# Kernel optimization log

Measured on AMD Instinct MI355X. Metric: run time of the kernel, lower is better.

The kernel has to match this reference:

```python
import jax, jax.numpy as jnp
import numpy as np

B, D, H, DH, NQ, NK = 64, 768, 8, 128, 256, 256


def _ln(x, g, b, eps=1e-5):
    m = x.mean(-1, keepdims=True)
    v = ((x - m) ** 2).mean(-1, keepdims=True)
    return (x - m) / jnp.sqrt(v + eps) * g + b


def setup_inputs() -> dict:
    key = jax.random.key(0)
    ks = jax.random.split(key, 16)
    w = lambda k, s: jax.random.normal(k, s, jnp.float32) * 0.02
    return {
        'emb_cause': jax.random.normal(ks[0], (B, D), jnp.float32),
        'emb_action': jax.random.normal(ks[1], (B, D), jnp.float32),
        'tok_cause': jax.random.normal(ks[2], (B, NK, D), jnp.float32),
        'tok_effect': jax.random.normal(ks[3], (B, NQ, D), jnp.float32),
        'fuse_ln_g': jnp.ones(2 * D), 'fuse_ln_b': jnp.zeros(2 * D),
        'fuse_w1': w(ks[4], (2 * D, D)), 'fuse_b1': jnp.zeros(D),
        'fuse_w2': w(ks[5], (D, D)), 'fuse_b2': jnp.zeros(D),
        'delta_ln_g': jnp.ones(D), 'delta_ln_b': jnp.zeros(D),
        'delta_w': w(ks[6], (D, D)), 'delta_b': jnp.zeros(D),
        'qg_w': w(ks[7], (D, H * DH)), 'qg_b': jnp.zeros(H * DH),
        'kg_w': w(ks[8], (D, H * DH)), 'kg_b': jnp.zeros(H * DH),
        'eff_ln_g': jnp.ones(D), 'eff_ln_b': jnp.zeros(D),
        'eff_w1': w(ks[9], (D, D)), 'eff_b1': jnp.zeros(D),
        'eff_w2': w(ks[10], (D, D)), 'eff_b2': jnp.zeros(D),
        'u_w': w(ks[11], (D, H * DH)),
        'v_w': w(ks[12], (D, H * DH)),
        'logit_scale': jnp.zeros(()),
    }


def reference(emb_cause, emb_action, tok_cause, tok_effect,
              fuse_ln_g, fuse_ln_b, fuse_w1, fuse_b1, fuse_w2, fuse_b2,
              delta_ln_g, delta_ln_b, delta_w, delta_b,
              qg_w, qg_b, kg_w, kg_b,
              eff_ln_g, eff_ln_b, eff_w1, eff_b1, eff_w2, eff_b2,
              u_w, v_w, logit_scale):
    # fuse: LN -> Linear -> GELU(exact) -> Linear (dropout = identity, eval)
    ctx_in = jnp.concatenate([emb_cause, emb_action], axis=-1)  # (B, 2D)
    h = jax.nn.gelu(_ln(ctx_in, fuse_ln_g, fuse_ln_b) @ fuse_w1 + fuse_b1, approximate=False)
    ctx = h @ fuse_w2 + fuse_b2  # (B, D)

    delta_e = _ln(ctx, delta_ln_g, delta_ln_b) @ delta_w + delta_b  # (B, D)
    pooled_effect = tok_effect.mean(axis=1)  # (B, D)
    e_shifted = pooled_effect + delta_e

    eh = jax.nn.gelu(_ln(ctx, eff_ln_g, eff_ln_b) @ eff_w1 + eff_b1, approximate=False)
    effect_pred = eh @ eff_w2 + eff_b2  # (B, D)

    q_gate = 1.0 + jnp.tanh(jax.nn.silu(ctx @ qg_w + qg_b)).reshape(B, H, DH)
    k_gate = 1.0 + jnp.tanh(jax.nn.silu(ctx @ kg_w + kg_b)).reshape(B, H, DH)

    # logit bias: torch code materializes (B,H,Nq,Nk,Dh); equivalent math is a
    # per-head inner product u.v (independent of q) broadcast over Nq.
    u = (e_shifted @ u_w).reshape(B, H, DH)            # (B, H, Dh)
    v = (tok_cause @ v_w).reshape(B, NK, H, DH)        # (B, Nk, H, Dh)
    bias = jnp.einsum('bhd,bkhd->bhk', u, v) / np.float32(np.sqrt(DH))
    logit_bias = jnp.exp(logit_scale) * jnp.broadcast_to(bias[:, :, None, :], (B, H, NQ, NK))

    return (q_gate, k_gate, e_shifted, delta_e, logit_bias, effect_pred)
```

## Files before the change

kernel.cpp:

```cpp
#include <hip/hip_runtime.h>
#include <math.h>

#define TPB 256

typedef float vf4 __attribute__((ext_vector_type(4)));

__device__ __forceinline__ float gelu_f(float x) {
    return 0.5f * x * (1.0f + erff(x * 0.70710678118654752f));
}
__device__ __forceinline__ float gate_f(float x) {
    float si = x / (1.0f + expf(-x));
    return 1.0f + tanhf(si);
}

template <class XL>
__device__ __forceinline__ void gemm_tile(XL xload, const float* __restrict__ W, int Wld, int cb,
                                          int k0, int kslice, float* part, int totN, int gcol, int s,
                                          float* __restrict__ xs, float* __restrict__ wt)
{
    const int t = threadIdx.x;
    const int tr4 = (t >> 4) << 2;
    const int tc4 = (t & 15) << 2;
    const int a  = t >> 5, kk = t & 31;
    const int wk = t >> 6, wc = t & 63;
    float xv[8], wv[8];
#pragma unroll
    for (int j = 0; j < 8; ++j) {
        xv[j] = xload(a + 8 * j, k0 + kk);
        wv[j] = W[(size_t)(k0 + wk + 4 * j) * Wld + cb + wc];
    }
    float acc[4][4] = {{0.f,0.f,0.f,0.f},{0.f,0.f,0.f,0.f},{0.f,0.f,0.f,0.f},{0.f,0.f,0.f,0.f}};
    for (int kc = 0; kc < kslice; kc += 32) {
#pragma unroll
        for (int j = 0; j < 8; ++j) {
            xs[kk * 68 + a + 8 * j] = xv[j];
            wt[(wk + 4 * j) * 68 + wc] = wv[j];
        }
        __syncthreads();
        int kn = kc + 32;
        if (kn < kslice) {
#pragma unroll
            for (int j = 0; j < 8; ++j) {
                xv[j] = xload(a + 8 * j, k0 + kn + kk);
                wv[j] = W[(size_t)(k0 + kn + wk + 4 * j) * Wld + cb + wc];
            }
        }
#pragma unroll
        for (int k = 0; k < 32; ++k) {
            float4 xq = *(const float4*)&xs[k * 68 + tr4];
            float4 wq = *(const float4*)&wt[k * 68 + tc4];
            acc[0][0] += xq.x * wq.x; acc[0][1] += xq.x * wq.y; acc[0][2] += xq.x * wq.z; acc[0][3] += xq.x * wq.w;
            acc[1][0] += xq.y * wq.x; acc[1][1] += xq.y * wq.y; acc[1][2] += xq.y * wq.z; acc[1][3] += xq.y * wq.w;
            acc[2][0] += xq.z * wq.x; acc[2][1] += xq.z * wq.y; acc[2][2] += xq.z * wq.z; acc[2][3] += xq.z * wq.w;
            acc[3][0] += xq.w * wq.x; acc[3][1] += xq.w * wq.y; acc[3][2] += xq.w * wq.z; acc[3][3] += xq.w * wq.w;
        }
        __syncthreads();
    }
    float* pp = part + (size_t)(s * 64 + tr4) * totN + gcol + tc4;
#pragma unroll
    for (int i = 0; i < 4; ++i)
#pragma unroll
        for (int j = 0; j < 4; ++j)
            pp[i * totN + j] = acc[i][j];
}

#define GEMM_LDS __shared__ float xs[32 * 68]; __shared__ float wt[32 * 68];

__device__ __forceinline__ void pool_task(const float* __restrict__ tok_effect,
                                          float* __restrict__ pp, int m, int t)
{
    int cch = m % 3, b = (m / 3) % 64, qz = m / 192;
    int c = cch * TPB + t;
    const float* base = tok_effect + (size_t)(b * 256 + qz * 64) * 768 + c;
    float s = 0.f;
#pragma unroll 16
    for (int q = 0; q < 64; ++q) s += __builtin_nontemporal_load(base + (size_t)q * 768);
    pp[(qz * 64 + b) * 768 + c] = s;
}

struct G1Args {
    const float *ec, *ea, *flg, *flb, *w1;
    const float *tok_effect;
    float *part1, *pp;
};
__global__ __launch_bounds__(256) void k_g1(G1Args A)
{
    GEMM_LDS;
    __shared__ float sred[8][64];
    __shared__ float sst[128];
    const int t = threadIdx.x;
    if (blockIdx.x >= 144) {
        pool_task(A.tok_effect, A.pp, blockIdx.x - 144, t);
        return;
    }
    {
        int row = t & 63, part = t >> 6;
        const float* src = (part < 2) ? (A.ec + row * 768 + part * 384)
                                      : (A.ea + row * 768 + (part - 2) * 384);
        const vf4* s4 = (const vf4*)src;
        float sum = 0.f, sq = 0.f;
#pragma unroll 8
        for (int j = 0; j < 96; ++j) {
            vf4 v = s4[j];
            sum += v.x + v.y + v.z + v.w;
            sq  += v.x * v.x + v.y * v.y + v.z * v.z + v.w * v.w;
        }
        sred[part][row] = sum;
        sred[4 + part][row] = sq;
        __syncthreads();
        if (t < 64) {
            float s = sred[0][t] + sred[1][t] + sred[2][t] + sred[3][t];
            float q = sred[4][t] + sred[5][t] + sred[6][t] + sred[7][t];
            float mean = s * (1.f / 1536.f);
            float var = q * (1.f / 1536.f) - mean * mean;
            sst[2 * t]     = mean;
            sst[2 * t + 1] = rsqrtf(var + 1e-5f);
        }
        __syncthreads();
    }
    int ct = blockIdx.x % 12, s = blockIdx.x / 12;
    auto xl = [&](int r, int k) {
        float raw = (k < 768) ? A.ec[r * 768 + k] : A.ea[r * 768 + (k - 768)];
        return (raw - sst[2 * r]) * sst[2 * r + 1] * A.flg[k] + A.flb[k];
    };
    gemm_tile(xl, A.w1, 768, ct * 64, s * 128, 128, A.part1, 768, ct * 64, s, xs, wt);
}

struct G2Args {
    const float *part1, *b1, *w2;
    const float *tok_effect;
    float *part2, *pp;
};
__global__ __launch_bounds__(256) void k_g2(G2Args A)
{
    GEMM_LDS;
    if (blockIdx.x >= 144) {
        pool_task(A.tok_effect, A.pp, blockIdx.x - 144 + 384, threadIdx.x);
        return;
    }
    int ct = blockIdx.x % 12, s = blockIdx.x / 12;
    auto xl = [&](int r, int k) {
        float v = A.b1[k];
#pragma unroll
        for (int q = 0; q < 12; ++q) v += A.part1[(size_t)(q * 64 + r) * 768 + k];
        return gelu_f(v);
    };
    gemm_tile(xl, A.w2, 768, ct * 64, s * 64, 64, A.part2, 768, ct * 64, s, xs, wt);
}

__global__ __launch_bounds__(256) void k_ln(const float* __restrict__ part2, const float* __restrict__ b2,
                                            float* __restrict__ ctx, float* __restrict__ stats2)
{
    int r = blockIdx.x, t = threadIdx.x;
    __shared__ float red[4];
    float v[3]; float sum = 0.f;
#pragma unroll
    for (int j = 0; j < 3; ++j) {
        int c = t + j * TPB;
        float x = b2[c];
#pragma unroll
        for (int s = 0; s < 12; ++s) x += part2[(size_t)(s * 64 + r) * 768 + c];
        v[j] = x; sum += x;
        ctx[r * 768 + c] = x;
    }
#pragma unroll
    for (int o_ = 32; o_ > 0; o_ >>= 1) sum += __shfl_xor(sum, o_);
    if ((t & 63) == 0) red[t >> 6] = sum;
    __syncthreads();
    sum = red[0] + red[1] + red[2] + red[3];
    float mean = sum * (1.f / 768.f);
    __syncthreads();
    float s2 = 0.f;
#pragma unroll
    for (int j = 0; j < 3; ++j) { float d = v[j] - mean; s2 += d * d; }
#pragma unroll
    for (int o_ = 32; o_ > 0; o_ >>= 1) s2 += __shfl_xor(s2, o_);
    if ((t & 63) == 0) red[t >> 6] = s2;
    __syncthreads();
    s2 = red[0] + red[1] + red[2] + red[3];
    if (t == 0) {
        stats2[2 * r]     = mean;
        stats2[2 * r + 1] = rsqrtf(s2 * (1.f / 768.f) + 1e-5f);
    }
}

struct GAArgs {
    const float *ctx, *stats2, *dg, *db, *eg, *eb;
    const float *delta_w, *eff_w1, *qg_w, *kg_w;
    const float *tok_cause;
    float* partA;
};
__global__ __launch_bounds__(256) void k_gA(GAArgs A)
{
    GEMM_LDS;
    if (blockIdx.x >= 448) {
        const vf4* tc = (const vf4*)A.tok_cause;
        unsigned idx = (blockIdx.x - 448) * TPB + threadIdx.x;
        for (unsigned i = idx; i < 3145728u; i += 320u * TPB) {
            vf4 v = tc[i];
            asm volatile("" :: "v"(v));
        }
        return;
    }
    int ct = blockIdx.x % 56, s = blockIdx.x / 56;
    if (ct < 12) {
        auto xl = [&](int r, int k) {
            float m = A.stats2[2 * r], rs = A.stats2[2 * r + 1];
            return (A.ctx[r * 768 + k] - m) * rs * A.dg[k] + A.db[k];
        };
        gemm_tile(xl, A.delta_w, 768, ct * 64, s * 96, 96, A.partA, 3584, ct * 64, s, xs, wt);
    } else if (ct < 24) {
        auto xl = [&](int r, int k) {
            float m = A.stats2[2 * r], rs = A.stats2[2 * r + 1];
            return (A.ctx[r * 768 + k] - m) * rs * A.eg[k] + A.eb[k];
        };
        gemm_tile(xl, A.eff_w1, 768, (ct - 12) * 64, s * 96, 96, A.partA, 3584, ct * 64, s, xs, wt);
    } else {
        auto xl = [&](int r, int k) { return A.ctx[r * 768 + k]; };
        const float* W = (ct < 40) ? A.qg_w : A.kg_w;
        int cb = (ct < 40) ? (ct - 24) * 64 : (ct - 40) * 64;
        gemm_tile(xl, W, 1024, cb, s * 96, 96, A.partA, 3584, ct * 64, s, xs, wt);
    }
}

struct MidArgs {
    const float *partA, *pp, *delta_b, *eff_b1, *qg_b, *kg_b, *eff_w2, *u_w;
    float *partB, *out_de, *out_es, *out_qg, *out_kg;
};
__global__ __launch_bounds__(256) void k_mid(MidArgs A)
{
    GEMM_LDS;
    const int t = threadIdx.x;
    if (blockIdx.x < 28) {
#pragma unroll
        for (int ii = 0; ii < 32; ++ii) {
            int idx = blockIdx.x * TPB + t + ii * 7168;
            int r = idx / 3584, c = idx - r * 3584;
            if (c >= 768 && c < 1536) continue;
            float v = 0.f;
#pragma unroll
            for (int q = 0; q < 8; ++q) v += A.partA[(size_t)(q * 64 + r) * 3584 + c];
            if (c < 768) {
                float de = v + A.delta_b[c];
                A.out_de[r * 768 + c] = de;
                float s4 = A.pp[r * 768 + c] + A.pp[(64 + r) * 768 + c]
                         + A.pp[(128 + r) * 768 + c] + A.pp[(192 + r) * 768 + c];
                A.out_es[r * 768 + c] = de + s4 * (1.f / 256.f);
            } else if (c < 2560) {
                A.out_qg[r * 1024 + (c - 1536)] = gate_f(v + A.qg_b[c - 1536]);
            } else {
                A.out_kg[r * 1024 + (c - 2560)] = gate_f(v + A.kg_b[c - 2560]);
            }
        }
    } else {
        int m = blockIdx.x - 28;
        int ct = m % 28, s = m / 28;
        if (ct < 12) {
            auto xl = [&](int r, int k) {
                float v = A.eff_b1[k];
#pragma unroll
                for (int q = 0; q < 8; ++q) v += A.partA[(size_t)(q * 64 + r) * 3584 + 768 + k];
                return gelu_f(v);
            };
            gemm_tile(xl, A.eff_w2, 768, ct * 64, s * 96, 96, A.partB, 1792, ct * 64, s, xs, wt);
        } else {
            auto xl = [&](int r, int k) {
                float v = A.delta_b[k];
#pragma unroll
                for (int q = 0; q < 8; ++q) v += A.partA[(size_t)(q * 64 + r) * 3584 + k];
                float s4 = A.pp[r * 768 + k] + A.pp[(64 + r) * 768 + k]
                         + A.pp[(128 + r) * 768 + k] + A.pp[(192 + r) * 768 + k];
                return v + s4 * (1.f / 256.f);
            };
            gemm_tile(xl, A.u_w, 1024, (ct - 12) * 64, s * 96, 96, A.partB, 1792, ct * 64, s, xs, wt);
        }
    }
}

__global__ __launch_bounds__(256) void k_tail(const float* __restrict__ partB, const float* __restrict__ eff_b2,
                                              const float* __restrict__ v_w,
                                              float* __restrict__ out_ep, float* __restrict__ wu)
{
    const int t = threadIdx.x;
    if (blockIdx.x < 6) {
#pragma unroll
        for (int ii = 0; ii < 32; ++ii) {
            int idx = blockIdx.x * TPB + t + ii * 1536;
            int r = idx / 768, c = idx - r * 768;
            float v = eff_b2[c];
#pragma unroll
            for (int q = 0; q < 8; ++q) v += partB[(size_t)(q * 64 + r) * 1792 + c];
            out_ep[r * 768 + c] = v;
        }
    } else {
        __shared__ float us[64 * 132];
        int m = blockIdx.x - 6;
        int h = m / 12, ctile = m % 12;
        for (int n = t; n < 8192; n += TPB) {
            int b = n >> 7, d = n & 127;
            float v = 0.f;
#pragma unroll
            for (int q = 0; q < 8; ++q) v += partB[(size_t)(q * 64 + b) * 1792 + 768 + h * 128 + d];
            us[b * 132 + d] = v;
        }
        __syncthreads();
        int c = ctile * 64 + (t >> 2);
        int bo = t & 3;
        const float* vr = v_w + (size_t)c * 1024 + h * 128;
        float acc[16];
#pragma unroll
        for (int i = 0; i < 16; ++i) acc[i] = 0.f;
        for (int d = 0; d < 128; d += 4) {
            float4 w4 = *(const float4*)(vr + d);
#pragma unroll
            for (int i = 0; i < 16; ++i) {
                const float* ub = &us[(4 * i + bo) * 132 + d];
                acc[i] += w4.x * ub[0] + w4.y * ub[1] + w4.z * ub[2] + w4.w * ub[3];
            }
        }
#pragma unroll
        for (int i = 0; i < 16; ++i) {
            int b = 4 * i + bo;
            wu[(b * 8 + h) * 768 + c] = acc[i];
        }
    }
}

__global__ __launch_bounds__(512) void k_biasbc(const float* __restrict__ tok_cause, const float* __restrict__ wu,
                         const float* __restrict__ ls_ptr, float* __restrict__ out_lb)
{
    int b = blockIdx.x, kt = blockIdx.y;
    __shared__ float wuh[8 * 768];
    __shared__ float bsm[8 * 32];
    for (int n = threadIdx.x; n < 6144; n += 512)
        wuh[n] = wu[b * 6144 + n];
    __syncthreads();
    const int lane = threadIdx.x & 63, w = threadIdx.x >> 6;
    vf4 wur[3][8];
#pragma unroll
    for (int j = 0; j < 3; ++j)
#pragma unroll
        for (int h = 0; h < 8; ++h)
            wur[j][h] = *(const vf4*)&wuh[h * 768 + (lane + 64 * j) * 4];
    float scale = expf(ls_ptr[0]) * 0.08838834764831845f;
#pragma unroll
    for (int rr = 0; rr < 4; ++rr) {
        int rl = w * 4 + rr;
        int row = kt * 32 + rl;
        const vf4* tr = (const vf4*)(tok_cause + ((size_t)b * 256 + row) * 768);
        vf4 t0 = tr[lane];
        vf4 t1 = tr[lane + 64];
        vf4 t2 = tr[lane + 128];
        float acc[8];
#pragma unroll
        for (int h = 0; h < 8; ++h) {
            acc[h] = t0.x * wur[0][h].x + t0.y * wur[0][h].y + t0.z * wur[0][h].z + t0.w * wur[0][h].w
                   + t1.x * wur[1][h].x + t1.y * wur[1][h].y + t1.z * wur[1][h].z + t1.w * wur[1][h].w
                   + t2.x * wur[2][h].x + t2.y * wur[2][h].y + t2.z * wur[2][h].z + t2.w * wur[2][h].w;
        }
#pragma unroll
        for (int h = 0; h < 8; ++h) {
            float vv = acc[h];
#pragma unroll
            for (int o_ = 32; o_ > 0; o_ >>= 1) vv += __shfl_xor(vv, o_);
            if (lane == 0) bsm[h * 32 + rl] = vv * scale;
        }
    }
    __syncthreads();
    const vf4* bs4 = (const vf4*)bsm;
    vf4* o4 = (vf4*)out_lb;
    int v = threadIdx.x & 7, sq0 = threadIdx.x >> 3;
#pragma unroll
    for (int it = 0; it < 32; ++it) {
        int seg = sq0 + it * 64;
        int h = seg >> 8, q = seg & 255;
        vf4 val = bs4[h * 8 + v];
        __builtin_nontemporal_store(val, &o4[(((size_t)(b * 8 + h) * 256 + q) << 6) + kt * 8 + v]);
    }
}

extern "C" void kernel_launch(void* const* d_in, const int* in_sizes, int n_in,
                              void* d_out, int out_size, void* d_ws, size_t ws_size,
                              hipStream_t stream)
{
    (void)in_sizes; (void)n_in; (void)out_size; (void)ws_size;
    const float* emb_cause  = (const float*)d_in[0];
    const float* emb_action = (const float*)d_in[1];
    const float* tok_cause  = (const float*)d_in[2];
    const float* tok_effect = (const float*)d_in[3];
    const float* fuse_ln_g  = (const float*)d_in[4];
    const float* fuse_ln_b  = (const float*)d_in[5];
    const float* fuse_w1    = (const float*)d_in[6];
    const float* fuse_b1    = (const float*)d_in[7];
    const float* fuse_w2    = (const float*)d_in[8];
    const float* fuse_b2    = (const float*)d_in[9];
    const float* delta_ln_g = (const float*)d_in[10];
    const float* delta_ln_b = (const float*)d_in[11];
    const float* delta_w    = (const float*)d_in[12];
    const float* delta_b    = (const float*)d_in[13];
    const float* qg_w       = (const float*)d_in[14];
    const float* qg_b       = (const float*)d_in[15];
    const float* kg_w       = (const float*)d_in[16];
    const float* kg_b       = (const float*)d_in[17];
    const float* eff_ln_g   = (const float*)d_in[18];
    const float* eff_ln_b   = (const float*)d_in[19];
    const float* eff_w1     = (const float*)d_in[20];
    const float* eff_b1     = (const float*)d_in[21];
    const float* eff_w2     = (const float*)d_in[22];
    const float* eff_b2     = (const float*)d_in[23];
    const float* u_w        = (const float*)d_in[24];
    const float* v_w        = (const float*)d_in[25];
    const float* logit_sc   = (const float*)d_in[26];

    float* ws = (float*)d_ws;
    float* ctx    = ws + 0;
    float* pp     = ws + 49152;
    float* wu     = ws + 245760;
    float* stats2 = ws + 638976;

    float* out    = (float*)d_out;
    float* out_qg = out + 0;
    float* out_kg = out + 65536;
    float* out_es = out + 131072;
    float* out_de = out + 180224;
    float* out_lb = out + 229376;
    float* out_ep = out + 33783808;

    float* pbase = out_lb + 20000000;
    float* part1 = pbase;
    float* part2 = pbase + 589824;
    float* partA = pbase + 1179648;
    float* partB = pbase + 3014656;

    {
        G1Args A; A.ec = emb_cause; A.ea = emb_action;
        A.flg = fuse_ln_g; A.flb = fuse_ln_b; A.w1 = fuse_w1;
        A.tok_effect = tok_effect; A.part1 = part1; A.pp = pp;
        k_g1<<<528, TPB, 0, stream>>>(A);
    }
    {
        G2Args A; A.part1 = part1; A.b1 = fuse_b1; A.w2 = fuse_w2;
        A.tok_effect = tok_effect; A.part2 = part2; A.pp = pp;
        k_g2<<<528, TPB, 0, stream>>>(A);
    }
    k_ln<<<64, TPB, 0, stream>>>(part2, fuse_b2, ctx, stats2);
    {
        GAArgs A; A.ctx = ctx; A.stats2 = stats2;
        A.dg = delta_ln_g; A.db = delta_ln_b; A.eg = eff_ln_g; A.eb = eff_ln_b;
        A.delta_w = delta_w; A.eff_w1 = eff_w1; A.qg_w = qg_w; A.kg_w = kg_w;
        A.tok_cause = tok_cause; A.partA = partA;
        k_gA<<<768, TPB, 0, stream>>>(A);
    }
    {
        MidArgs M; M.partA = partA; M.pp = pp;
        M.delta_b = delta_b; M.eff_b1 = eff_b1; M.qg_b = qg_b; M.kg_b = kg_b;
        M.eff_w2 = eff_w2; M.u_w = u_w; M.partB = partB;
        M.out_de = out_de; M.out_es = out_es; M.out_qg = out_qg; M.out_kg = out_kg;
        k_mid<<<252, TPB, 0, stream>>>(M);
    }
    k_tail<<<102, TPB, 0, stream>>>(partB, eff_b2, v_w, out_ep, wu);
    k_biasbc<<<dim3(64, 8), 512, 0, stream>>>(tok_cause, wu, logit_sc, out_lb);
}
```

Baseline: 155.8 us.

## Fold LayerNorm statistics out of GEMMs and drop the separate LN kernel

Rewrites each LayerNorm-then-Linear as a GEMM on gamma-scaled raw inputs, applying mean and rstd afterwards through precomputed gamma@W and beta@W vectors. Row statistics come from extra blocks running alongside the GEMMs, so the k_ln launch and the ctx buffer go away and ctx is rebuilt from partials inside k_gA. The tok_cause L2 prefetch blocks are removed. The cost is redundant reloads of part2 partials in every GEMM tile, a slow serial K-loop for the weight-vector products, and E[x^2]-mean^2 variance, which is less numerically stable.

```diff
diff --git a/kernel.cpp b/kernel.cpp
--- a/kernel.cpp
+++ b/kernel.cpp
@@ -80,54 +80,65 @@
 
 struct G1Args {
     const float *ec, *ea, *flg, *flb, *w1;
+    const float *dg, *db, *eg, *eb, *delta_w, *eff_w1;
     const float *tok_effect;
-    float *part1, *pp;
+    float *part1, *pp, *stats1, *gW1, *bW1, *dgW, *dbW, *egW, *ebW;
 };
 __global__ __launch_bounds__(256) void k_g1(G1Args A)
 {
     GEMM_LDS;
-    __shared__ float sred[8][64];
-    __shared__ float sst[128];
+    __shared__ float red[8];
     const int t = threadIdx.x;
-    if (blockIdx.x >= 144) {
+    if (blockIdx.x < 144) {
+        int ct = blockIdx.x % 12, s = blockIdx.x / 12;
+        auto xl = [&](int r, int k) {
+            float raw = (k < 768) ? A.ec[r * 768 + k] : A.ea[r * 768 + (k - 768)];
+            return raw * A.flg[k];
+        };
+        gemm_tile(xl, A.w1, 768, ct * 64, s * 128, 128, A.part1, 768, ct * 64, s, xs, wt);
+    } else if (blockIdx.x < 528) {
         pool_task(A.tok_effect, A.pp, blockIdx.x - 144, t);
-        return;
-    }
-    {
-        int row = t & 63, part = t >> 6;
-        const float* src = (part < 2) ? (A.ec + row * 768 + part * 384)
-                                      : (A.ea + row * 768 + (part - 2) * 384);
-        const vf4* s4 = (const vf4*)src;
+    } else if (blockIdx.x < 592) {
+        int r = blockIdx.x - 528;
         float sum = 0.f, sq = 0.f;
-#pragma unroll 8
-        for (int j = 0; j < 96; ++j) {
-            vf4 v = s4[j];
-            sum += v.x + v.y + v.z + v.w;
-            sq  += v.x * v.x + v.y * v.y + v.z * v.z + v.w * v.w;
-        }
-        sred[part][row] = sum;
-        sred[4 + part][row] = sq;
+#pragma unroll
+        for (int j = 0; j < 6; ++j) {
+            int c = t + j * TPB;
+            float x = (c < 768) ? A.ec[r * 768 + c] : A.ea[r * 768 + (c - 768)];
+            sum += x; sq += x * x;
+        }
+#pragma unroll
+        for (int o_ = 32; o_ > 0; o_ >>= 1) { sum += __shfl_xor(sum, o_); sq += __shfl_xor(sq, o_); }
+        if ((t & 63) == 0) { red[t >> 6] = sum; red[4 + (t >> 6)] = sq; }
         __syncthreads();
-        if (t < 64) {
-            float s = sred[0][t] + sred[1][t] + sred[2][t] + sred[3][t];
-            float q = sred[4][t] + sred[5][t] + sred[6][t] + sred[7][t];
+        if (t == 0) {
+            float s = red[0] + red[1] + red[2] + red[3];
+            float q = red[4] + red[5] + red[6] + red[7];
             float mean = s * (1.f / 1536.f);
-            float var = q * (1.f / 1536.f) - mean * mean;
-            sst[2 * t]     = mean;
-            sst[2 * t + 1] = rsqrtf(var + 1e-5f);
-        }
-        __syncthreads();
-    }
-    int ct = blockIdx.x % 12, s = blockIdx.x / 12;
-    auto xl = [&](int r, int k) {
-        float raw = (k < 768) ? A.ec[r * 768 + k] : A.ea[r * 768 + (k - 768)];
-        return (raw - sst[2 * r]) * sst[2 * r + 1] * A.flg[k] + A.flb[k];
-    };
-    gemm_tile(xl, A.w1, 768, ct * 64, s * 128, 128, A.part1, 768, ct * 64, s, xs, wt);
+            A.stats1[2 * r]     = mean;
+            A.stats1[2 * r + 1] = rsqrtf(q * (1.f / 1536.f) - mean * mean + 1e-5f);
+        }
+    } else {
+        int m = blockIdx.x - 592;
+        int id = m / 3, chunk = m % 3;
+        const float* vec; const float* W; int K; float* out;
+        switch (id) {
+            case 0: vec = A.flg; W = A.w1;      K = 1536; out = A.gW1; break;
+            case 1: vec = A.flb; W = A.w1;      K = 1536; out = A.bW1; break;
+            case 2: vec = A.dg;  W = A.delta_w; K = 768;  out = A.dgW; break;
+            case 3: vec = A.db;  W = A.delta_w; K = 768;  out = A.dbW; break;
+            case 4: vec = A.eg;  W = A.eff_w1;  K = 768;  out = A.egW; break;
+            default: vec = A.eb; W = A.eff_w1;  K = 768;  out = A.ebW; break;
+        }
+        int col = chunk * TPB + t;
+        float acc = 0.f;
+        for (int c = 0; c < K; ++c) acc += vec[c] * W[(size_t)c * 768 + col];
+        out[col] = acc;
+    }
 }
 
 struct G2Args {
-    const float *part1, *b1, *w2;
+    const float *part1, *b1, *w2, *stats1, *gW1, *bW1;
     const float *tok_effect;
     float *part2, *pp;
 };
@@ -140,83 +151,64 @@
     }
     int ct = blockIdx.x % 12, s = blockIdx.x / 12;
     auto xl = [&](int r, int k) {
-        float v = A.b1[k];
+        float v = 0.f;
 #pragma unroll
         for (int q = 0; q < 12; ++q) v += A.part1[(size_t)(q * 64 + r) * 768 + k];
-        return gelu_f(v);
+        float m = A.stats1[2 * r], rs = A.stats1[2 * r + 1];
+        return gelu_f(rs * (v - m * A.gW1[k]) + A.bW1[k] + A.b1[k]);
     };
     gemm_tile(xl, A.w2, 768, ct * 64, s * 64, 64, A.part2, 768, ct * 64, s, xs, wt);
 }
 
-__global__ __launch_bounds__(256) void k_ln(const float* __restrict__ part2, const float* __restrict__ b2,
-                                            float* __restrict__ ctx, float* __restrict__ stats2)
-{
-    int r = blockIdx.x, t = threadIdx.x;
-    __shared__ float red[4];
-    float v[3]; float sum = 0.f;
-#pragma unroll
-    for (int j = 0; j < 3; ++j) {
-        int c = t + j * TPB;
-        float x = b2[c];
-#pragma unroll
-        for (int s = 0; s < 12; ++s) x += part2[(size_t)(s * 64 + r) * 768 + c];
-        v[j] = x; sum += x;
-        ctx[r * 768 + c] = x;
-    }
-#pragma unroll
-    for (int o_ = 32; o_ > 0; o_ >>= 1) sum += __shfl_xor(sum, o_);
-    if ((t & 63) == 0) red[t >> 6] = sum;
-    __syncthreads();
-    sum = red[0] + red[1] + red[2] + red[3];
-    float mean = sum * (1.f / 768.f);
-    __syncthreads();
-    float s2 = 0.f;
-#pragma unroll
-    for (int j = 0; j < 3; ++j) { float d = v[j] - mean; s2 += d * d; }
-#pragma unroll
-    for (int o_ = 32; o_ > 0; o_ >>= 1) s2 += __shfl_xor(s2, o_);
-    if ((t & 63) == 0) red[t >> 6] = s2;
-    __syncthreads();
-    s2 = red[0] + red[1] + red[2] + red[3];
-    if (t == 0) {
-        stats2[2 * r]     = mean;
-        stats2[2 * r + 1] = rsqrtf(s2 * (1.f / 768.f) + 1e-5f);
-    }
-}
-
 struct GAArgs {
-    const float *ctx, *stats2, *dg, *db, *eg, *eb;
+    const float *part2, *b2, *dg, *eg;
     const float *delta_w, *eff_w1, *qg_w, *kg_w;
-    const float *tok_cause;
-    float* partA;
+    float *partA, *stats2;
 };
 __global__ __launch_bounds__(256) void k_gA(GAArgs A)
 {
     GEMM_LDS;
+    __shared__ float red[8];
+    const int t = threadIdx.x;
     if (blockIdx.x >= 448) {
-        const vf4* tc = (const vf4*)A.tok_cause;
-        unsigned idx = (blockIdx.x - 448) * TPB + threadIdx.x;
-        for (unsigned i = idx; i < 3145728u; i += 320u * TPB) {
-            vf4 v = tc[i];
-            asm volatile("" :: "v"(v));
+        int r = blockIdx.x - 448;
+        float sum = 0.f, sq = 0.f;
+#pragma unroll
+        for (int j = 0; j < 3; ++j) {
+            int c = t + j * TPB;
+            float x = A.b2[c];
+#pragma unroll
+            for (int q = 0; q < 12; ++q) x += A.part2[(size_t)(q * 64 + r) * 768 + c];
+            sum += x; sq += x * x;
+        }
+#pragma unroll
+        for (int o_ = 32; o_ > 0; o_ >>= 1) { sum += __shfl_xor(sum, o_); sq += __shfl_xor(sq, o_); }
+        if ((t & 63) == 0) { red[t >> 6] = sum; red[4 + (t >> 6)] = sq; }
+        __syncthreads();
+        if (t == 0) {
+            float s = red[0] + red[1] + red[2] + red[3];
+            float q = red[4] + red[5] + red[6] + red[7];
+            float mean = s * (1.f / 768.f);
+            A.stats2[2 * r]     = mean;
+            A.stats2[2 * r + 1] = rsqrtf(q * (1.f / 768.f) - mean * mean + 1e-5f);
         }
         return;
     }
     int ct = blockIdx.x % 56, s = blockIdx.x / 56;
+    auto ctxv = [&](int r, int k) {
+        float v = A.b2[k];
+#pragma unroll
+        for (int q = 0; q < 12; ++q) v += A.part2[(size_t)(q * 64 + r) * 768 + k];
+        return v;
+    };
     if (ct < 12) {
-        auto xl = [&](int r, int k) {
-            float m = A.stats2[2 * r], rs = A.stats2[2 * r + 1];
-            return (A.ctx[r * 768 + k] - m) * rs * A.dg[k] + A.db[k];
-        };
+        auto xl = [&](int r, int k) { return ctxv(r, k) * A.dg[k]; };
         gemm_tile(xl, A.delta_w, 768, ct * 64, s * 96, 96, A.partA, 3584, ct * 64, s, xs, wt);
     } else if (ct < 24) {
-        auto xl = [&](int r, int k) {
-            float m = A.stats2[2 * r], rs = A.stats2[2 * r + 1];
-            return (A.ctx[r * 768 + k] - m) * rs * A.eg[k] + A.eb[k];
-        };
+        auto xl = [&](int r, int k) { return ctxv(r, k) * A.eg[k]; };
         gemm_tile(xl, A.eff_w1, 768, (ct - 12) * 64, s * 96, 96, A.partA, 3584, ct * 64, s, xs, wt);
     } else {
-        auto xl = [&](int r, int k) { return A.ctx[r * 768 + k]; };
+        auto xl = [&](int r, int k) { return ctxv(r, k); };
         const float* W = (ct < 40) ? A.qg_w : A.kg_w;
         int cb = (ct < 40) ? (ct - 24) * 64 : (ct - 40) * 64;
         gemm_tile(xl, W, 1024, cb, s * 96, 96, A.partA, 3584, ct * 64, s, xs, wt);
@@ -224,7 +216,8 @@
 }
 
 struct MidArgs {
-    const float *partA, *pp, *delta_b, *eff_b1, *qg_b, *kg_b, *eff_w2, *u_w;
+    const float *partA, *pp, *stats2, *dgW, *dbW, *egW, *ebW;
+    const float *delta_b, *eff_b1, *qg_b, *kg_b, *eff_w2, *u_w;
     float *partB, *out_de, *out_es, *out_qg, *out_kg;
 };
 __global__ __launch_bounds__(256) void k_mid(MidArgs A)
@@ -241,7 +234,8 @@
 #pragma unroll
             for (int q = 0; q < 8; ++q) v += A.partA[(size_t)(q * 64 + r) * 3584 + c];
             if (c < 768) {
-                float de = v + A.delta_b[c];
+                float m = A.stats2[2 * r], rs = A.stats2[2 * r + 1];
+                float de = rs * (v - m * A.dgW[c]) + A.dbW[c] + A.delta_b[c];
                 A.out_de[r * 768 + c] = de;
                 float s4 = A.pp[r * 768 + c] + A.pp[(64 + r) * 768 + c]
                          + A.pp[(128 + r) * 768 + c] + A.pp[(192 + r) * 768 + c];
@@ -257,20 +251,23 @@
         int ct = m % 28, s = m / 28;
         if (ct < 12) {
             auto xl = [&](int r, int k) {
-                float v = A.eff_b1[k];
+                float v = 0.f;
 #pragma unroll
                 for (int q = 0; q < 8; ++q) v += A.partA[(size_t)(q * 64 + r) * 3584 + 768 + k];
-                return gelu_f(v);
+                float mm = A.stats2[2 * r], rs = A.stats2[2 * r + 1];
+                return gelu_f(rs * (v - mm * A.egW[k]) + A.ebW[k] + A.eff_b1[k]);
             };
             gemm_tile(xl, A.eff_w2, 768, ct * 64, s * 96, 96, A.partB, 1792, ct * 64, s, xs, wt);
         } else {
             auto xl = [&](int r, int k) {
-                float v = A.delta_b[k];
+                float v = 0.f;
 #pragma unroll
                 for (int q = 0; q < 8; ++q) v += A.partA[(size_t)(q * 64 + r) * 3584 + k];
+                float mm = A.stats2[2 * r], rs = A.stats2[2 * r + 1];
+                float de = rs * (v - mm * A.dgW[k]) + A.dbW[k] + A.delta_b[k];
                 float s4 = A.pp[r * 768 + k] + A.pp[(64 + r) * 768 + k]
                          + A.pp[(128 + r) * 768 + k] + A.pp[(192 + r) * 768 + k];
-                return v + s4 * (1.f / 256.f);
+                return de + s4 * (1.f / 256.f);
             };
             gemm_tile(xl, A.u_w, 1024, (ct - 12) * 64, s * 96, 96, A.partB, 1792, ct * 64, s, xs, wt);
         }
@@ -413,10 +410,16 @@
     const float* logit_sc   = (const float*)d_in[26];
 
     float* ws = (float*)d_ws;
-    float* ctx    = ws + 0;
-    float* pp     = ws + 49152;
-    float* wu     = ws + 245760;
-    float* stats2 = ws + 638976;
+    float* pp     = ws + 0;
+    float* wu     = ws + 196608;
+    float* stats1 = ws + 589824;
+    float* stats2 = ws + 589952;
+    float* gW1    = ws + 590080;
+    float* bW1    = ws + 590848;
+    float* dgW    = ws + 591616;
+    float* dbW    = ws + 592384;
+    float* egW    = ws + 593152;
+    float* ebW    = ws + 593920;
 
     float* out    = (float*)d_out;
     float* out_qg = out + 0;
@@ -435,24 +438,29 @@
     {
         G1Args A; A.ec = emb_cause; A.ea = emb_action;
         A.flg = fuse_ln_g; A.flb = fuse_ln_b; A.w1 = fuse_w1;
-        A.tok_effect = tok_effect; A.part1 = part1; A.pp = pp;
-        k_g1<<<528, TPB, 0, stream>>>(A);
+        A.dg = delta_ln_g; A.db = delta_ln_b; A.eg = eff_ln_g; A.eb = eff_ln_b;
+        A.delta_w = delta_w; A.eff_w1 = eff_w1;
+        A.tok_effect = tok_effect;
+        A.part1 = part1; A.pp = pp; A.stats1 = stats1;
+        A.gW1 = gW1; A.bW1 = bW1; A.dgW = dgW; A.dbW = dbW; A.egW = egW; A.ebW = ebW;
+        k_g1<<<610, TPB, 0, stream>>>(A);
     }
     {
         G2Args A; A.part1 = part1; A.b1 = fuse_b1; A.w2 = fuse_w2;
+        A.stats1 = stats1; A.gW1 = gW1; A.bW1 = bW1;
         A.tok_effect = tok_effect; A.part2 = part2; A.pp = pp;
         k_g2<<<528, TPB, 0, stream>>>(A);
     }
-    k_ln<<<64, TPB, 0, stream>>>(part2, fuse_b2, ctx, stats2);
     {
-        GAArgs A; A.ctx = ctx; A.stats2 = stats2;
-        A.dg = delta_ln_g; A.db = delta_ln_b; A.eg = eff_ln_g; A.eb = eff_ln_b;
+        GAArgs A; A.part2 = part2; A.b2 = fuse_b2;
+        A.dg = delta_ln_g; A.eg = eff_ln_g;
         A.delta_w = delta_w; A.eff_w1 = eff_w1; A.qg_w = qg_w; A.kg_w = kg_w;
-        A.tok_cause = tok_cause; A.partA = partA;
-        k_gA<<<768, TPB, 0, stream>>>(A);
+        A.partA = partA; A.stats2 = stats2;
+        k_gA<<<512, TPB, 0, stream>>>(A);
     }
     {
-        MidArgs M; M.partA = partA; M.pp = pp;
+        MidArgs M; M.partA = partA; M.pp = pp; M.stats2 = stats2;
+        M.dgW = dgW; M.dbW = dbW; M.egW = egW; M.ebW = ebW;
         M.delta_b = delta_b; M.eff_b1 = eff_b1; M.qg_b = qg_b; M.kg_b = kg_b;
         M.eff_w2 = eff_w2; M.u_w = u_w; M.partB = partB;
         M.out_de = out_de; M.out_es = out_es; M.out_qg = out_qg; M.out_kg = out_kg;
```

Measured after the change: 500.1 us. 3.21x slower.
